# Performance work log

Hardware: AMD Instinct MI355X
Metric: run time of the kernel (lower is better)

The kernel has to match this reference:

```python
import jax, jax.numpy as jnp
import numpy as np

B = 8192
CNN_DIM = 2048
MLP_DIM = 2048
HID = 1024
H = 16
D = HID // H  # 64
EPS = 1e-5


def setup_inputs() -> dict:
    key = jax.random.key(0)
    ks = jax.random.split(key, 12)
    s = 0.02
    return {
        'cnn_out': jax.random.normal(ks[0], (B, CNN_DIM), jnp.float32),
        'mlp_out': jax.random.normal(ks[1], (B, MLP_DIM), jnp.float32),
        # weights stored [in, out] (transposed vs torch nn.Linear)
        'W_cqkv': jax.random.normal(ks[2], (CNN_DIM, 3 * HID), jnp.float32) * s,
        'b_cqkv': jnp.zeros((3 * HID,), jnp.float32),
        'W_mqkv': jax.random.normal(ks[3], (MLP_DIM, 3 * HID), jnp.float32) * s,
        'b_mqkv': jnp.zeros((3 * HID,), jnp.float32),
        'g1': jnp.ones((HID,), jnp.float32),
        'be1': jnp.zeros((HID,), jnp.float32),
        'g2': jnp.ones((HID,), jnp.float32),
        'be2': jnp.zeros((HID,), jnp.float32),
        'W_cproj': jax.random.normal(ks[4], (HID, CNN_DIM), jnp.float32) * s,
        'b_cproj': jnp.zeros((CNN_DIM,), jnp.float32),
        'W_mproj': jax.random.normal(ks[5], (HID, MLP_DIM), jnp.float32) * s,
        'b_mproj': jnp.zeros((MLP_DIM,), jnp.float32),
    }


def _layernorm(x, g, b):
    m = jnp.mean(x, axis=-1, keepdims=True)
    v = jnp.mean((x - m) ** 2, axis=-1, keepdims=True)
    return (x - m) / jnp.sqrt(v + EPS) * g + b


def reference(cnn_out, mlp_out, W_cqkv, b_cqkv, W_mqkv, b_mqkv,
              g1, be1, g2, be2, W_cproj, b_cproj, W_mproj, b_mproj):
    bsz = cnn_out.shape[0]
    scale = 1.0 / jnp.sqrt(jnp.float32(D))

    cqkv = (cnn_out @ W_cqkv + b_cqkv).reshape(bsz, 3, H, D)
    cq, ck, cv = cqkv[:, 0], cqkv[:, 1], cqkv[:, 2]  # each [B,H,D]
    mqkv = (mlp_out @ W_mqkv + b_mqkv).reshape(bsz, 3, H, D)
    mq, mk, mv = mqkv[:, 0], mqkv[:, 1], mqkv[:, 2]

    # branch 1: cnn queries attend over mlp heads -> [B,H,H]
    a1 = jax.nn.softmax(jnp.einsum('bhd,bgd->bhg', cq, mk) * scale, axis=-1)
    ca = jnp.einsum('bhg,bgd->bhd', a1, mv)
    # torch: transpose(1,2).view(B, hidden) -> [B, D, H] flattened
    ca = jnp.swapaxes(ca, 1, 2).reshape(bsz, HID)
    cnn_enh = cnn_out + _layernorm(ca, g1, be1) @ W_cproj + b_cproj

    # branch 2: mlp queries attend over cnn heads
    a2 = jax.nn.softmax(jnp.einsum('bhd,bgd->bhg', mq, ck) * scale, axis=-1)
    ma = jnp.einsum('bhg,bgd->bhd', a2, cv)
    ma = jnp.swapaxes(ma, 1, 2).reshape(bsz, HID)
    mlp_enh = mlp_out + _layernorm(ma, g2, be2) @ W_mproj + b_mproj

    return (cnn_enh, mlp_enh)
```

## Files before the change

kernel.cpp:

```cpp
#include <hip/hip_runtime.h>
#include <hip/hip_bf16.h>
#include <cstdint>
#include <cstddef>

#define NROWS 8192
#define DIM   2048
#define HIDN  1024
#define QKV3  3072
#define EPSV  1e-5f

typedef __attribute__((ext_vector_type(8))) short bf16x8;
typedef __attribute__((ext_vector_type(4))) float f32x4;

__device__ __forceinline__ unsigned short f2bf(float x) {
    __hip_bfloat16 h = __float2bfloat16(x);
    return *reinterpret_cast<unsigned short*>(&h);
}
__device__ __forceinline__ float bf2f(unsigned short u) {
    return __uint_as_float((unsigned)u << 16);
}

__device__ __forceinline__ void gload_lds16(const void* g, void* l) {
    __builtin_amdgcn_global_load_lds(
        (const __attribute__((address_space(1))) void*)g,
        (__attribute__((address_space(3))) void*)l, 16, 0, 0);
}

template <int N> __device__ __forceinline__ void vmwait() {
    if constexpr (N == 16)     asm volatile("s_waitcnt vmcnt(16)" ::: "memory");
    else if constexpr (N == 8) asm volatile("s_waitcnt vmcnt(8)" ::: "memory");
    else if constexpr (N == 4) asm volatile("s_waitcnt vmcnt(4)" ::: "memory");
    else if constexpr (N == 0) asm volatile("s_waitcnt vmcnt(0)" ::: "memory");
}
__device__ __forceinline__ void barrier_mem() {
    asm volatile("s_barrier" ::: "memory");
}

__global__ __launch_bounds__(256) void prep(
    const float* __restrict__ cnn, unsigned short* __restrict__ Abf_c,
    const float* __restrict__ mlp, unsigned short* __restrict__ Abf_m,
    const float* __restrict__ Wcq, unsigned short* __restrict__ WqT_c,
    const float* __restrict__ Wmq, unsigned short* __restrict__ WqT_m,
    const float* __restrict__ Wcp, unsigned short* __restrict__ WpT_c,
    const float* __restrict__ Wmp, unsigned short* __restrict__ WpT_m) {
    __shared__ float tile[32][33];
    const int bid = blockIdx.x;
    const int t = threadIdx.x;
    if (bid < 16384) {
        const int which = bid >> 13;
        const long b = bid & 8191;
        const float* in = which ? mlp : cnn;
        unsigned short* out = which ? Abf_m : Abf_c;
        const long base = (b * 256 + t) * 8;
        float4 a = *(const float4*)(in + base);
        float4 v = *(const float4*)(in + base + 4);
        uint4 r;
        r.x = (unsigned)f2bf(a.x) | ((unsigned)f2bf(a.y) << 16);
        r.y = (unsigned)f2bf(a.z) | ((unsigned)f2bf(a.w) << 16);
        r.z = (unsigned)f2bf(v.x) | ((unsigned)f2bf(v.y) << 16);
        r.w = (unsigned)f2bf(v.z) | ((unsigned)f2bf(v.w) << 16);
        *(uint4*)(out + base) = r;
        return;
    }
    const int tx = t & 31, ty = t >> 5;
    const float* in;
    unsigned short* out;
    int R, C, l, gw;
    if (bid < 28672) {
        l = bid - 16384;
        const int wq = l / 6144;
        l -= wq * 6144;
        in = wq ? Wmq : Wcq; out = wq ? WqT_m : WqT_c; R = DIM; C = QKV3; gw = 96;
    } else {
        l = bid - 28672;
        const int wp = l / 2048;
        l -= wp * 2048;
        in = wp ? Wmp : Wcp; out = wp ? WpT_m : WpT_c; R = HIDN; C = DIM; gw = 64;
    }
    const int c0 = (l % gw) * 32, r0 = (l / gw) * 32;
#pragma unroll
    for (int i = 0; i < 4; ++i)
        tile[ty + i * 8][tx] = in[(size_t)(r0 + ty + i * 8) * C + c0 + tx];
    __syncthreads();
#pragma unroll
    for (int i = 0; i < 4; ++i)
        out[(size_t)(c0 + ty + i * 8) * R + r0 + tx] = f2bf(tile[tx][ty + i * 8]);
}


__device__ __forceinline__ void stage_half(const unsigned short* __restrict__ G,
                                           int ldK, int rowBase, int kt,
                                           short* ldsHalf, int tid) {
#pragma unroll
    for (int i = 0; i < 4; ++i) {
        const int c = i * 256 + tid;
        const int r = c >> 3;
        const int jl = (c & 7) ^ (r & 7);
        const unsigned short* src = G + (size_t)(rowBase + r) * ldK + kt + jl * 8;
        char* dst = (char*)ldsHalf + (size_t)((i * 256 + (tid & 0xC0)) * 16);
        gload_lds16(src, dst);
    }
}

__device__ __forceinline__ void load_f4(const short* base, int rowOff, int o0,
                                        int tbase, bf16x8 (&d)[4][2]) {
#pragma unroll
    for (int m = 0; m < 4; ++m) {
        const char* p = (const char*)base + rowOff + (tbase + m) * 4096;
        d[m][0] = *(const bf16x8*)(p + o0);
        d[m][1] = *(const bf16x8*)(p + (o0 ^ 64));
    }
}

#define QUAD(mq, nq, BSET)                                                    \
    __builtin_amdgcn_s_setprio(1);                                            \
    _Pragma("unroll") for (int kk_ = 0; kk_ < 2; ++kk_)                       \
    _Pragma("unroll") for (int n_ = 0; n_ < 4; ++n_)                          \
    _Pragma("unroll") for (int m_ = 0; m_ < 4; ++m_)                          \
        acc[(mq) + m_][(nq) + n_] = __builtin_amdgcn_mfma_f32_16x16x32_bf16(  \
            a[m_][kk_], BSET[n_][kk_], acc[(mq) + m_][(nq) + n_], 0, 0, 0);   \
    __builtin_amdgcn_s_setprio(0);

#define KTILE(BUF, MODE, KT1, KT2)                                            \
                                                                     \
    if constexpr ((MODE) <= 1)                                                \
        stage_half(Bt, K, tn + 128, (KT1), &sB[(BUF) ^ 1][8192], tid);        \
    if constexpr ((MODE) == 2) { vmwait<4>(); } else { vmwait<16>(); }        \
    barrier_mem();                                                            \
    QUAD(0, 0, bL);                                                           \
                                                                     \
    load_f4(&sB[BUF][0], rowB, o0, 4, bH);                                    \
    if constexpr ((MODE) <= 1)                                                \
        stage_half(A, K, tm + 128, (KT1), &sA[(BUF) ^ 1][8192], tid);         \
    if constexpr ((MODE) == 2) { vmwait<0>(); } else { vmwait<16>(); }        \
    barrier_mem();                                                            \
    QUAD(0, 4, bH);                                                           \
                                                                     \
    load_f4(&sA[BUF][0], rowA, o0, 4, a);                                     \
    if constexpr ((MODE) == 0)                                                \
        stage_half(A, K, tm, (KT2), &sA[BUF][0], tid);                        \
    barrier_mem();                                                            \
    QUAD(4, 4, bH);                                                           \
                                                                     \
    if constexpr ((MODE) == 0) {                                              \
        stage_half(Bt, K, tn, (KT2), &sB[BUF][0], tid);                       \
        vmwait<16>();                                                         \
    }                                                                         \
    if constexpr ((MODE) == 1) { vmwait<8>(); }                               \
    barrier_mem();                                                            \
    QUAD(4, 0, bL);                                                           \
    if constexpr ((MODE) <= 1) {                                              \
        load_f4(&sA[(BUF) ^ 1][0], rowA, o0, 0, a);             \
        load_f4(&sB[(BUF) ^ 1][0], rowB, o0, 0, bL);            \
    }

template <int EPI>
__global__ __launch_bounds__(256, 1) void gemm256(
    const unsigned short* __restrict__ A0, const unsigned short* __restrict__ B0t,
    const float* __restrict__ bias0, const float* __restrict__ res0, void* __restrict__ C0,
    const unsigned short* __restrict__ A1, const unsigned short* __restrict__ B1t,
    const float* __restrict__ bias1, const float* __restrict__ res1, void* __restrict__ C1,
    int M, int N, int K, int nbx) {
    __shared__ __align__(16) short sA[2][16384];
    __shared__ __align__(16) short sB[2][16384];

    const int tid = threadIdx.x;
    const int nwg = gridDim.x;
    const int ob = blockIdx.x;
    const int swz = (ob & 7) * (nwg >> 3) + (ob >> 3);
    const int per = nbx * (M >> 8);
    const int which = swz >= per ? 1 : 0;
    const int rem = swz - which * per;
    const int by = rem / nbx, bx = rem % nbx;
    const int tm = by << 8, tn = bx << 8;

    const unsigned short* __restrict__ A  = which ? A1 : A0;
    const unsigned short* __restrict__ Bt = which ? B1t : B0t;
    const float* __restrict__ bias  = which ? bias1 : bias0;
    const float* __restrict__ resid = which ? res1 : res0;

    const int w = tid >> 6, l = tid & 63;
    const int wm = w >> 1, wn = w & 1;
    const int lg = l >> 4, lr = l & 15;
    const int o0 = (lg ^ (lr & 7)) << 4;
    const int rowA = (16 * wm + lr) << 7;
    const int rowB = (16 * wn + lr) << 7;

    f32x4 acc[8][8] = {};
    bf16x8 a[4][2], bL[4][2], bH[4][2];

    const int T = K >> 6;

    stage_half(A,  K, tm,       0,  &sA[0][0],    tid);
    stage_half(Bt, K, tn,       0,  &sB[0][0],    tid);
    stage_half(Bt, K, tn + 128, 0,  &sB[0][8192], tid);
    stage_half(A,  K, tm + 128, 0,  &sA[0][8192], tid);
    stage_half(A,  K, tm,       64, &sA[1][0],    tid);
    stage_half(Bt, K, tn,       64, &sB[1][0],    tid);
    vmwait<16>();
    barrier_mem();
    load_f4(&sA[0][0], rowA, o0, 0, a);
    load_f4(&sB[0][0], rowB, o0, 0, bL);

    int kt = 0;
    for (int tt = 0; tt + 4 <= T; tt += 2) {
        KTILE(0, 0, kt + 64, kt + 128);
        KTILE(1, 0, kt + 128, kt + 192);
        kt += 128;
    }
    KTILE(0, 1, kt + 64, 0);
    KTILE(1, 2, 0, 0);

    const int crow0 = tm + 16 * wm + 4 * lg;
    const int ccol0 = tn + 16 * wn + lr;
    if constexpr (EPI == 0) {
        unsigned short* C = (unsigned short*)(which ? C1 : C0);
#pragma unroll
        for (int mi = 0; mi < 8; ++mi) {
            const int r0 = crow0 + 32 * mi;
#pragma unroll
            for (int ni = 0; ni < 8; ++ni) {
                const int col = ccol0 + 32 * ni;
                const float bb = bias[col];
#pragma unroll
                for (int j = 0; j < 4; ++j)
                    C[(size_t)(r0 + j) * N + col] = f2bf(acc[mi][ni][j] + bb);
            }
        }
    } else {
        float* C = (float*)(which ? C1 : C0);
#pragma unroll
        for (int mi = 0; mi < 8; ++mi) {
            const int r0 = crow0 + 32 * mi;
#pragma unroll
            for (int ni = 0; ni < 8; ++ni) {
                const int col = ccol0 + 32 * ni;
                const float bb = bias[col];
#pragma unroll
                for (int j = 0; j < 4; ++j) {
                    const size_t idx = (size_t)(r0 + j) * N + col;
                    C[idx] = acc[mi][ni][j] + bb + resid[idx];
                }
            }
        }
    }
}

__device__ __forceinline__ void attn_path(const float* __restrict__ q,
                                          const float* __restrict__ k,
                                          const float* __restrict__ v,
                                          const float* __restrict__ gw,
                                          const float* __restrict__ bw,
                                          unsigned short* __restrict__ out, long b,
                                          float* sS, float* sP, float* red, int t) {
    const int h = t >> 4, gg = t & 15;
    const float* qr = q + h * 65;
    const float* kr = k + gg * 65;
    float s = 0.f;
#pragma unroll
    for (int d = 0; d < 64; ++d) s += qr[d] * kr[d];
    sS[t] = s * 0.125f;
    __syncthreads();
    float mx = -1e30f;
#pragma unroll
    for (int j = 0; j < 16; ++j) mx = fmaxf(mx, sS[h * 16 + j]);
    float sum = 0.f;
#pragma unroll
    for (int j = 0; j < 16; ++j) sum += __expf(sS[h * 16 + j] - mx);
    const float aa = __expf(sS[t] - mx) / sum;
    sP[t] = aa;
    __syncthreads();
    float xs[4];
    float lsum = 0.f, lss = 0.f;
#pragma unroll
    for (int r = 0; r < 4; ++r) {
        const int i = t + 256 * r;
        const int d = i >> 4, hh = i & 15;
        float accv = 0.f;
#pragma unroll
        for (int g2 = 0; g2 < 16; ++g2) accv += sP[hh * 16 + g2] * v[g2 * 65 + d];
        xs[r] = accv;
        lsum += accv;
        lss += accv * accv;
    }
#pragma unroll
    for (int off = 32; off > 0; off >>= 1) {
        lsum += __shfl_down(lsum, off);
        lss += __shfl_down(lss, off);
    }
    if ((t & 63) == 0) {
        red[(t >> 6) * 2] = lsum;
        red[(t >> 6) * 2 + 1] = lss;
    }
    __syncthreads();
    const float tot = red[0] + red[2] + red[4] + red[6];
    const float tot2 = red[1] + red[3] + red[5] + red[7];
    const float mean = tot * (1.f / 1024.f);
    const float var = tot2 * (1.f / 1024.f) - mean * mean;
    const float rstd = rsqrtf(var + EPSV);
#pragma unroll
    for (int r = 0; r < 4; ++r) {
        const int i = t + 256 * r;
        const float y = (xs[r] - mean) * rstd * gw[i] + bw[i];
        out[b * 1024 + i] = f2bf(y);
    }
}

__global__ __launch_bounds__(256) void attn_ln(const unsigned short* __restrict__ qkv_c,
                                               const unsigned short* __restrict__ qkv_m,
                                               const float* __restrict__ g1,
                                               const float* __restrict__ be1,
                                               const float* __restrict__ g2,
                                               const float* __restrict__ be2,
                                               unsigned short* __restrict__ ln1,
                                               unsigned short* __restrict__ ln2) {
    __shared__ float qc[48 * 65];
    __shared__ float qm[48 * 65];
    __shared__ float sS[256];
    __shared__ float sP[256];
    __shared__ float red[8];
    const int t = threadIdx.x;
    const long b = blockIdx.x;

    const unsigned short* rc = qkv_c + b * QKV3;
    const unsigned short* rm = qkv_m + b * QKV3;
#pragma unroll
    for (int it = 0; it < 3; ++it) {
        const int i0 = t * 4 + it * 1024;
        ushort4 vc = *(const ushort4*)(rc + i0);
        ushort4 vm = *(const ushort4*)(rm + i0);
        const int o = i0 + (i0 >> 6);
        qc[o + 0] = bf2f(vc.x); qc[o + 1] = bf2f(vc.y);
        qc[o + 2] = bf2f(vc.z); qc[o + 3] = bf2f(vc.w);
        qm[o + 0] = bf2f(vm.x); qm[o + 1] = bf2f(vm.y);
        qm[o + 2] = bf2f(vm.z); qm[o + 3] = bf2f(vm.w);
    }
    __syncthreads();
    attn_path(qc, qm + 16 * 65, qm + 32 * 65, g1, be1, ln1, b, sS, sP, red, t);
    __syncthreads();
    attn_path(qm, qc + 16 * 65, qc + 32 * 65, g2, be2, ln2, b, sS, sP, red, t);
}

extern "C" void kernel_launch(void* const* d_in, const int* in_sizes, int n_in,
                              void* d_out, int out_size, void* d_ws, size_t ws_size,
                              hipStream_t stream) {
    const float* cnn    = (const float*)d_in[0];
    const float* mlp    = (const float*)d_in[1];
    const float* W_cqkv = (const float*)d_in[2];
    const float* b_cqkv = (const float*)d_in[3];
    const float* W_mqkv = (const float*)d_in[4];
    const float* b_mqkv = (const float*)d_in[5];
    const float* g1     = (const float*)d_in[6];
    const float* be1    = (const float*)d_in[7];
    const float* g2     = (const float*)d_in[8];
    const float* be2    = (const float*)d_in[9];
    const float* W_cproj = (const float*)d_in[10];
    const float* b_cproj = (const float*)d_in[11];
    const float* W_mproj = (const float*)d_in[12];
    const float* b_mproj = (const float*)d_in[13];
    float* out = (float*)d_out;
    char* ws = (char*)d_ws;

    unsigned short* Abf_c = (unsigned short*)(ws + 0);
    unsigned short* Abf_m = (unsigned short*)(ws + 33554432);
    unsigned short* WqT_c = (unsigned short*)(ws + 67108864);
    unsigned short* WqT_m = (unsigned short*)(ws + 79691776);
    unsigned short* qkv_c = (unsigned short*)(ws + 92274688);
    unsigned short* qkv_m = (unsigned short*)(ws + 142606336);
    unsigned short* ln1   = (unsigned short*)(ws + 0);
    unsigned short* ln2   = (unsigned short*)(ws + 16777216);
    unsigned short* WpT_c = (unsigned short*)(ws + 192937984);
    unsigned short* WpT_m = (unsigned short*)(ws + 197132288);

    prep<<<32768, 256, 0, stream>>>(cnn, Abf_c, mlp, Abf_m,
                                    W_cqkv, WqT_c, W_mqkv, WqT_m,
                                    W_cproj, WpT_c, W_mproj, WpT_m);

    gemm256<0><<<768, 256, 0, stream>>>(Abf_c, WqT_c, b_cqkv, nullptr, qkv_c,
                                        Abf_m, WqT_m, b_mqkv, nullptr, qkv_m,
                                        NROWS, QKV3, DIM, QKV3 / 256);

    attn_ln<<<NROWS, 256, 0, stream>>>(qkv_c, qkv_m, g1, be1, g2, be2, ln1, ln2);

    gemm256<1><<<512, 256, 0, stream>>>(ln1, WpT_c, b_cproj, cnn, out,
                                        ln2, WpT_m, b_mproj, mlp, out + (size_t)NROWS * DIM,
                                        NROWS, DIM, HIDN, DIM / 256);
}
```

Baseline: 468.3 us.

## Use 8 waves per GEMM workgroup with 256x256 tile split into 8x4 accumulators

```diff
diff --git a/kernel.cpp b/kernel.cpp
--- a/kernel.cpp
+++ b/kernel.cpp
@@ -27,9 +27,9 @@
 }
 
 template <int N> __device__ __forceinline__ void vmwait() {
-    if constexpr (N == 16)     asm volatile("s_waitcnt vmcnt(16)" ::: "memory");
-    else if constexpr (N == 8) asm volatile("s_waitcnt vmcnt(8)" ::: "memory");
+    if constexpr (N == 8)      asm volatile("s_waitcnt vmcnt(8)" ::: "memory");
     else if constexpr (N == 4) asm volatile("s_waitcnt vmcnt(4)" ::: "memory");
+    else if constexpr (N == 2) asm volatile("s_waitcnt vmcnt(2)" ::: "memory");
     else if constexpr (N == 0) asm volatile("s_waitcnt vmcnt(0)" ::: "memory");
 }
 __device__ __forceinline__ void barrier_mem() {
@@ -92,70 +92,80 @@
                                            int ldK, int rowBase, int kt,
                                            short* ldsHalf, int tid) {
 #pragma unroll
-    for (int i = 0; i < 4; ++i) {
-        const int c = i * 256 + tid;
+    for (int i = 0; i < 2; ++i) {
+        const int c = i * 512 + tid;
         const int r = c >> 3;
         const int jl = (c & 7) ^ (r & 7);
         const unsigned short* src = G + (size_t)(rowBase + r) * ldK + kt + jl * 8;
-        char* dst = (char*)ldsHalf + (size_t)((i * 256 + (tid & 0xC0)) * 16);
+        char* dst = (char*)ldsHalf + (size_t)((i * 512 + (tid & 0x1C0)) * 16);
         gload_lds16(src, dst);
     }
 }
 
-__device__ __forceinline__ void load_f4(const short* base, int rowOff, int o0,
-                                        int tbase, bf16x8 (&d)[4][2]) {
+__device__ __forceinline__ void load_a4(const short* sAb, int rowA, int o0, int mbase,
+                                        bf16x8 (&d)[4][2]) {
 #pragma unroll
     for (int m = 0; m < 4; ++m) {
-        const char* p = (const char*)base + rowOff + (tbase + m) * 4096;
+        const char* p = (const char*)sAb + rowA + (mbase + m) * 4096;
         d[m][0] = *(const bf16x8*)(p + o0);
         d[m][1] = *(const bf16x8*)(p + (o0 ^ 64));
     }
 }
-
-#define QUAD(mq, nq, BSET)                                                    \
+__device__ __forceinline__ void load_b2(const short* sBb, int rowB, int o0, int nbase,
+                                        bf16x8 (&b)[4][2]) {
+#pragma unroll
+    for (int n = 0; n < 2; ++n) {
+        const char* p = (const char*)sBb + rowB + (nbase + n) * 8192;
+        b[nbase + n][0] = *(const bf16x8*)(p + o0);
+        b[nbase + n][1] = *(const bf16x8*)(p + (o0 ^ 64));
+    }
+}
+
+#define QUAD(ASET, mq, nq)                                                    \
     __builtin_amdgcn_s_setprio(1);                                            \
     _Pragma("unroll") for (int kk_ = 0; kk_ < 2; ++kk_)                       \
-    _Pragma("unroll") for (int n_ = 0; n_ < 4; ++n_)                          \
+    _Pragma("unroll") for (int n_ = 0; n_ < 2; ++n_)                          \
     _Pragma("unroll") for (int m_ = 0; m_ < 4; ++m_)                          \
         acc[(mq) + m_][(nq) + n_] = __builtin_amdgcn_mfma_f32_16x16x32_bf16(  \
-            a[m_][kk_], BSET[n_][kk_], acc[(mq) + m_][(nq) + n_], 0, 0, 0);   \
+            ASET[m_][kk_], b[(nq) + n_][kk_], acc[(mq) + m_][(nq) + n_],      \
+            0, 0, 0);                                                         \
     __builtin_amdgcn_s_setprio(0);
 
 #define KTILE(BUF, MODE, KT1, KT2)                                            \
-                                                                     \
+                              \
     if constexpr ((MODE) <= 1)                                                \
         stage_half(Bt, K, tn + 128, (KT1), &sB[(BUF) ^ 1][8192], tid);        \
-    if constexpr ((MODE) == 2) { vmwait<4>(); } else { vmwait<16>(); }        \
+    if constexpr ((MODE) == 2) { vmwait<2>(); } else { vmwait<8>(); }         \
     barrier_mem();                                                            \
-    QUAD(0, 0, bL);                                                           \
-                                                                     \
-    load_f4(&sB[BUF][0], rowB, o0, 4, bH);                                    \
+    load_b2(&sB[BUF][0], rowB, o0, 2, b);                                     \
+    QUAD(aL, 0, 0);                                                           \
+                               \
     if constexpr ((MODE) <= 1)                                                \
         stage_half(A, K, tm + 128, (KT1), &sA[(BUF) ^ 1][8192], tid);         \
-    if constexpr ((MODE) == 2) { vmwait<0>(); } else { vmwait<16>(); }        \
+    if constexpr ((MODE) == 2) { vmwait<0>(); } else { vmwait<8>(); }         \
     barrier_mem();                                                            \
-    QUAD(0, 4, bH);                                                           \
-                                                                     \
-    load_f4(&sA[BUF][0], rowA, o0, 4, a);                                     \
+    load_a4(&sA[BUF][0], rowA, o0, 4, aH);                                    \
+    QUAD(aL, 0, 2);                                                           \
+                                             \
     if constexpr ((MODE) == 0)                                                \
         stage_half(A, K, tm, (KT2), &sA[BUF][0], tid);                        \
     barrier_mem();                                                            \
-    QUAD(4, 4, bH);                                                           \
-                                                                     \
+    QUAD(aH, 4, 0);                                                           \
+                   \
     if constexpr ((MODE) == 0) {                                              \
         stage_half(Bt, K, tn, (KT2), &sB[BUF][0], tid);                       \
-        vmwait<16>();                                                         \
+        vmwait<8>();                                                          \
     }                                                                         \
-    if constexpr ((MODE) == 1) { vmwait<8>(); }                               \
+    if constexpr ((MODE) == 1) { vmwait<4>(); }                               \
     barrier_mem();                                                            \
-    QUAD(4, 0, bL);                                                           \
     if constexpr ((MODE) <= 1) {                                              \
-        load_f4(&sA[(BUF) ^ 1][0], rowA, o0, 0, a);             \
-        load_f4(&sB[(BUF) ^ 1][0], rowB, o0, 0, bL);            \
-    }
+        load_a4(&sA[(BUF) ^ 1][0], rowA, o0, 0, aL);                          \
+        load_b2(&sB[(BUF) ^ 1][0], rowB, o0, 0, b);                           \
+    }                                                                         \
+    QUAD(aH, 4, 2);
 
 template <int EPI>
-__global__ __launch_bounds__(256, 1) void gemm256(
+__global__ __launch_bounds__(512, 2) void gemm256(
     const unsigned short* __restrict__ A0, const unsigned short* __restrict__ B0t,
     const float* __restrict__ bias0, const float* __restrict__ res0, void* __restrict__ C0,
     const unsigned short* __restrict__ A1, const unsigned short* __restrict__ B1t,
@@ -180,14 +190,14 @@
     const float* __restrict__ resid = which ? res1 : res0;
 
     const int w = tid >> 6, l = tid & 63;
-    const int wm = w >> 1, wn = w & 1;
+    const int wm = w >> 2, wn = w & 3;
     const int lg = l >> 4, lr = l & 15;
     const int o0 = (lg ^ (lr & 7)) << 4;
     const int rowA = (16 * wm + lr) << 7;
     const int rowB = (16 * wn + lr) << 7;
 
-    f32x4 acc[8][8] = {};
-    bf16x8 a[4][2], bL[4][2], bH[4][2];
+    f32x4 acc[8][4] = {};
+    bf16x8 aL[4][2], aH[4][2], b[4][2];
 
     const int T = K >> 6;
 
@@ -197,10 +207,10 @@
     stage_half(A,  K, tm + 128, 0,  &sA[0][8192], tid);
     stage_half(A,  K, tm,       64, &sA[1][0],    tid);
     stage_half(Bt, K, tn,       64, &sB[1][0],    tid);
-    vmwait<16>();
+    vmwait<8>();
     barrier_mem();
-    load_f4(&sA[0][0], rowA, o0, 0, a);
-    load_f4(&sB[0][0], rowB, o0, 0, bL);
+    load_a4(&sA[0][0], rowA, o0, 0, aL);
+    load_b2(&sB[0][0], rowB, o0, 0, b);
 
     int kt = 0;
     for (int tt = 0; tt + 4 <= T; tt += 2) {
@@ -219,8 +229,8 @@
         for (int mi = 0; mi < 8; ++mi) {
             const int r0 = crow0 + 32 * mi;
 #pragma unroll
-            for (int ni = 0; ni < 8; ++ni) {
-                const int col = ccol0 + 32 * ni;
+            for (int ni = 0; ni < 4; ++ni) {
+                const int col = ccol0 + 64 * ni;
                 const float bb = bias[col];
 #pragma unroll
                 for (int j = 0; j < 4; ++j)
@@ -233,8 +243,8 @@
         for (int mi = 0; mi < 8; ++mi) {
             const int r0 = crow0 + 32 * mi;
 #pragma unroll
-            for (int ni = 0; ni < 8; ++ni) {
-                const int col = ccol0 + 32 * ni;
+            for (int ni = 0; ni < 4; ++ni) {
+                const int col = ccol0 + 64 * ni;
                 const float bb = bias[col];
 #pragma unroll
                 for (int j = 0; j < 4; ++j) {
@@ -376,13 +386,13 @@
                                     W_cqkv, WqT_c, W_mqkv, WqT_m,
                                     W_cproj, WpT_c, W_mproj, WpT_m);
 
-    gemm256<0><<<768, 256, 0, stream>>>(Abf_c, WqT_c, b_cqkv, nullptr, qkv_c,
+    gemm256<0><<<768, 512, 0, stream>>>(Abf_c, WqT_c, b_cqkv, nullptr, qkv_c,
                                         Abf_m, WqT_m, b_mqkv, nullptr, qkv_m,
                                         NROWS, QKV3, DIM, QKV3 / 256);
 
     attn_ln<<<NROWS, 256, 0, stream>>>(qkv_c, qkv_m, g1, be1, g2, be2, ln1, ln2);
 
-    gemm256<1><<<512, 256, 0, stream>>>(ln1, WpT_c, b_cproj, cnn, out,
+    gemm256<1><<<512, 512, 0, stream>>>(ln1, WpT_c, b_cproj, cnn, out,
                                         ln2, WpT_m, b_mproj, mlp, out + (size_t)NROWS * DIM,
                                         NROWS, DIM, HIDN, DIM / 256);
 }
```

Result: slower. 769.6 us (+64.3%).
